# Kernel optimization log

Hardware: AMD Instinct MI355X
Metric: run time of the kernel (lower is better)

Reference implementation:

```python
import jax, jax.numpy as jnp
import numpy as np

N, E, DIN, DH, DOUT = 100000, 1600000, 512, 128, 40


def setup_inputs() -> dict:
    key = jax.random.key(0)
    ks = jax.random.split(key, 4)
    x = jax.random.normal(ks[0], (N, DIN), dtype=jnp.float32)
    edge_index = jax.random.randint(ks[1], (2, E), 0, N, dtype=jnp.int32)
    W1 = jax.random.normal(ks[2], (DIN, DH), dtype=jnp.float32) / np.sqrt(DIN).astype(np.float32)
    b1 = jnp.zeros((DH,), jnp.float32)
    W2 = jax.random.normal(ks[3], (DH, DOUT), dtype=jnp.float32) / np.sqrt(DH).astype(np.float32)
    b2 = jnp.zeros((DOUT,), jnp.float32)
    return {"x": x, "edge_index": edge_index, "W1": W1, "b1": b1, "W2": W2, "b2": b2}


def _gcn_conv(x, W, b, src, dst, norm, n):
    # PyG GCNConv: linear transform first, then normalized neighbor aggregation
    h = x @ W                                   # [n, d_out]
    msg = h[src] * norm[:, None]                # gather + scale, [E+n, d_out]
    out = jax.ops.segment_sum(msg, dst, num_segments=n)  # scatter-add
    return out + b


def reference(x, edge_index, W1, b1, W2, b2):
    n = x.shape[0]
    loops = jnp.arange(n, dtype=edge_index.dtype)
    src = jnp.concatenate([edge_index[0], loops])   # with self-loops
    dst = jnp.concatenate([edge_index[1], loops])
    deg = jax.ops.segment_sum(jnp.ones_like(dst, dtype=jnp.float32), dst, num_segments=n)
    dinv = jnp.where(deg > 0, jax.lax.rsqrt(jnp.maximum(deg, 1.0)), 0.0)
    norm = dinv[src] * dinv[dst]                    # deg^{-1/2}[j] * deg^{-1/2}[i]
    h = jax.nn.relu(_gcn_conv(x, W1, b1, src, dst, norm, n))
    # dropout p=0.5 is a no-op in eval mode (training=False)
    h = _gcn_conv(h, W2, b2, src, dst, norm, n)
    return h, jax.nn.log_softmax(h, axis=1)
```

## Files before the change

### kernel.cpp

```cpp
#include <hip/hip_runtime.h>
#include <math.h>


typedef unsigned int uint;
typedef unsigned short ushort_t;
using short8  = __attribute__((ext_vector_type(8))) short;
using float4v = __attribute__((ext_vector_type(4))) float;

__device__ __forceinline__ ushort_t f2bf(float f) {
    uint u = __float_as_uint(f);
    u += 0x7FFFu + ((u >> 16) & 1u);
    return (ushort_t)(u >> 16);
}
__device__ __forceinline__ float2 unpack2(uint v) {
    return make_float2(__uint_as_float(v << 16), __uint_as_float(v & 0xFFFF0000u));
}
__device__ __forceinline__ uint pack2(float a, float b) {
    return (uint)f2bf(a) | ((uint)f2bf(b) << 16);
}


__global__ __launch_bounds__(256) void k_bhist(const int* __restrict__ dst,
                                               int* __restrict__ bcnt, int e, int nb) {
    __shared__ int h[800];
    for (int t = threadIdx.x; t < nb; t += 256) h[t] = 0;
    __syncthreads();
    int ibase = blockIdx.x * 2560 + threadIdx.x;
#pragma unroll
    for (int j = 0; j < 10; j++) {
        int i = ibase + j * 256;
        if (i < e) atomicAdd(&h[dst[i] >> 7], 1);
    }
    __syncthreads();
    for (int t = threadIdx.x; t < nb; t += 256) {
        int c = h[t];
        if (c) atomicAdd(&bcnt[t], c);
    }
}

__global__ __launch_bounds__(256) void k_bscan(const int* __restrict__ bcnt, int* __restrict__ bbase,
                                               int* __restrict__ bcur, int* __restrict__ row_ptr,
                                               int nb, int n, int e) {
    __shared__ int sd[256];
    int t = threadIdx.x;
    int base = t * 4;
    int v[4];
#pragma unroll
    for (int j = 0; j < 4; j++) v[j] = (base + j < nb) ? bcnt[base + j] : 0;
    int s0 = v[0], s1 = s0 + v[1], s2 = s1 + v[2], s3 = s2 + v[3];
    sd[t] = s3;
    __syncthreads();
    for (int d = 1; d < 256; d <<= 1) {
        int x = (t >= d) ? sd[t - d] : 0;
        __syncthreads();
        sd[t] += x;
        __syncthreads();
    }
    int excl = sd[t] - s3;
    int pre0 = excl, pre1 = excl + s0, pre2 = excl + s1, pre3 = excl + s2;
    if (base + 0 < nb) { bbase[base + 0] = pre0; bcur[base + 0] = pre0; }
    if (base + 1 < nb) { bbase[base + 1] = pre1; bcur[base + 1] = pre1; }
    if (base + 2 < nb) { bbase[base + 2] = pre2; bcur[base + 2] = pre2; }
    if (base + 3 < nb) { bbase[base + 3] = pre3; bcur[base + 3] = pre3; }
    if (t == 255) bbase[nb] = excl + s3;
    if (t == 0) row_ptr[n] = e;
}

__global__ __launch_bounds__(256) void k_part(const int* __restrict__ src, const int* __restrict__ dst,
                                              int* __restrict__ bcur, uint* __restrict__ pbuf,
                                              int e, int nb) {
    __shared__ int h[800];
    __shared__ int base_l[800];
    for (int t = threadIdx.x; t < nb; t += 256) h[t] = 0;
    __syncthreads();
    uint pk[10]; int bk[10]; int lp[10];
    int ibase = blockIdx.x * 2560 + threadIdx.x;
#pragma unroll
    for (int j = 0; j < 10; j++) {
        int i = ibase + j * 256;
        bk[j] = -1;
        if (i < e) {
            int s = src[i], d = dst[i];
            int b = d >> 7;
            bk[j] = b;
            pk[j] = ((uint)(d & 127) << 25) | (uint)s;
            lp[j] = atomicAdd(&h[b], 1);
        }
    }
    __syncthreads();
    for (int t = threadIdx.x; t < nb; t += 256) {
        int c = h[t];
        base_l[t] = c ? atomicAdd(&bcur[t], c) : 0;
    }
    __syncthreads();
#pragma unroll
    for (int j = 0; j < 10; j++) {
        if (bk[j] >= 0) pbuf[base_l[bk[j]] + lp[j]] = pk[j];
    }
}

__global__ __launch_bounds__(256) void k_bsort(const uint* __restrict__ pbuf,
                                               const int* __restrict__ bbase,
                                               int* __restrict__ cnt,
                                               int* __restrict__ row_ptr,
                                               int* __restrict__ es_src, int n) {
    __shared__ int cl[128];
    __shared__ int cur[128];
    const int b = blockIdx.x;
    const int tid = threadIdx.x;
    const int ebeg = bbase[b], eend = bbase[b + 1];
    const int m = eend - ebeg;
    if (tid < 128) cl[tid] = 0;
    __syncthreads();
    for (int i = tid; i < m; i += 256) {
        uint p = pbuf[ebeg + i];
        atomicAdd(&cl[p >> 25], 1);
    }
    __syncthreads();
    int own = (tid < 128) ? cl[tid] : 0;
    for (int d = 1; d < 128; d <<= 1) {
        int v = 0;
        if (tid < 128 && tid >= d) v = cl[tid - d];
        __syncthreads();
        if (tid < 128 && tid >= d) cl[tid] += v;
        __syncthreads();
    }
    if (tid < 128) {
        int excl = cl[tid] - own;
        int node = b * 128 + tid;
        if (node < n) {
            cnt[node] = own;
            row_ptr[node] = ebeg + excl;
        }
        cur[tid] = excl;
    }
    __syncthreads();
    for (int i = tid; i < m; i += 256) {
        uint p = pbuf[ebeg + i];
        int dl = (int)(p >> 25);
        int pos = atomicAdd(&cur[dl], 1);
        es_src[ebeg + pos] = (int)(p & 0x1FFFFFFu);
    }
}

__global__ void k_dinv(const int* __restrict__ cnt, float* __restrict__ dinv, int n) {
    int i = blockIdx.x * blockDim.x + threadIdx.x;
    if (i < n) dinv[i] = rsqrtf((float)(cnt[i] + 1));
}

__global__ __launch_bounds__(256) void k_w1t(const float* __restrict__ W1, ushort_t* __restrict__ W1t) {
    int idx = blockIdx.x * 256 + threadIdx.x;
    int nn = idx >> 9, k = idx & 511;
    W1t[idx] = f2bf(W1[(size_t)k * 128 + nn]);
}

__global__ __launch_bounds__(256) void k_w2t(const float* __restrict__ W2, ushort_t* __restrict__ W2t) {
    int idx = blockIdx.x * 256 + threadIdx.x;
    if (idx >= 6144) return;
    int c = idx >> 7, k = idx & 127;
    W2t[idx] = (c < 40) ? f2bf(W2[(size_t)k * 40 + c]) : (ushort_t)0;
}

__global__ __launch_bounds__(256) void k_gemm1(const float* __restrict__ x,
                                               const ushort_t* __restrict__ W1t,
                                               const float* __restrict__ dinv,
                                               ushort_t* __restrict__ h, int n) {
    __shared__ ushort_t As[64][72];
    __shared__ ushort_t Bs[128][72];
    const int tid  = threadIdx.x;
    const int w    = tid >> 6, lane = tid & 63;
    const int quad = lane >> 4, l16 = lane & 15;
    const int row0 = blockIdx.x * 64;

    float4v acc[8];
#pragma unroll
    for (int i = 0; i < 8; i++) acc[i] = (float4v)0.f;

    const int ar  = tid >> 2;
    const int akq = (tid & 3) * 16;
    const int br  = tid >> 1;
    const int bkq = (tid & 1) * 32;
    const int agrow = row0 + ar;
    const float* xp0 = &x[(size_t)agrow * 512];
    const ushort_t* wp0 = &W1t[(size_t)br * 512];

    for (int kb = 0; kb < 512; kb += 64) {
#pragma unroll
        for (int j = 0; j < 4; j++) {
            float4 v = make_float4(0.f, 0.f, 0.f, 0.f);
            if (agrow < n) v = *(const float4*)(xp0 + kb + akq + j * 4);
            ushort4 b;
            b.x = f2bf(v.x); b.y = f2bf(v.y); b.z = f2bf(v.z); b.w = f2bf(v.w);
            *(ushort4*)&As[ar][akq + j * 4] = b;
        }
#pragma unroll
        for (int j = 0; j < 8; j++) {
            *(ushort4*)&Bs[br][bkq + j * 4] = *(const ushort4*)(wp0 + kb + bkq + j * 4);
        }
        __syncthreads();
#pragma unroll
        for (int ks = 0; ks < 64; ks += 32) {
            short8 a = *(const short8*)&As[w * 16 + l16][ks + quad * 8];
#pragma unroll
            for (int ct = 0; ct < 8; ct++) {
                short8 b = *(const short8*)&Bs[ct * 16 + l16][ks + quad * 8];
                acc[ct] = __builtin_amdgcn_mfma_f32_16x16x32_bf16(a, b, acc[ct], 0, 0, 0);
            }
        }
        __syncthreads();
    }
#pragma unroll
    for (int r = 0; r < 4; r++) {
        int grow = row0 + w * 16 + quad * 4 + r;
        if (grow >= n) continue;
        float di = dinv[grow];
#pragma unroll
        for (int ct = 0; ct < 8; ct++) {
            int col = ct * 16 + l16;
            h[(size_t)grow * 128 + col] = f2bf(di * acc[ct][r]);
        }
    }
}

__global__ __launch_bounds__(256) void k_agg1(const uint* __restrict__ h,
                                              const int* __restrict__ row_ptr,
                                              const int* __restrict__ es_src,
                                              const float* __restrict__ dinv,
                                              const float* __restrict__ b1,
                                              uint* __restrict__ h1, int n) {
    const int tid  = threadIdx.x;
    const int node = blockIdx.x * 4 + (tid >> 6);
    if (node >= n) return;
    const int lane = tid & 63;
    float2 acc = unpack2(h[(size_t)node * 64 + lane]);
    const int k0 = row_ptr[node], k1 = row_ptr[node + 1];
    int k = k0;
    for (; k + 3 < k1; k += 4) {
        int s0 = es_src[k], s1 = es_src[k + 1], s2 = es_src[k + 2], s3 = es_src[k + 3];
        float2 v0 = unpack2(h[(size_t)s0 * 64 + lane]);
        float2 v1 = unpack2(h[(size_t)s1 * 64 + lane]);
        float2 v2 = unpack2(h[(size_t)s2 * 64 + lane]);
        float2 v3 = unpack2(h[(size_t)s3 * 64 + lane]);
        acc.x += (v0.x + v1.x) + (v2.x + v3.x);
        acc.y += (v0.y + v1.y) + (v2.y + v3.y);
    }
    for (; k < k1; k++) {
        int s = es_src[k];
        float2 v = unpack2(h[(size_t)s * 64 + lane]);
        acc.x += v.x;
        acc.y += v.y;
    }
    const float di = dinv[node];
    float2 bb = *(const float2*)&b1[lane * 2];
    acc.x = di * acc.x + bb.x;
    acc.y = di * acc.y + bb.y;
    acc.x = acc.x > 0.f ? acc.x : 0.f;
    acc.y = acc.y > 0.f ? acc.y : 0.f;
    h1[(size_t)node * 64 + lane] = pack2(acc.x, acc.y);
}

__global__ __launch_bounds__(256) void k_gemm2(const ushort_t* __restrict__ h1,
                                               const ushort_t* __restrict__ W2t,
                                               const float* __restrict__ dinv,
                                               float* __restrict__ g, int n) {
    __shared__ ushort_t As[64][136];
    __shared__ ushort_t Bs[48][136];
    const int tid  = threadIdx.x;
    const int w    = tid >> 6, lane = tid & 63;
    const int quad = lane >> 4, l16 = lane & 15;
    const int row0 = blockIdx.x * 64;

    {
        int ar = tid >> 2;
        int ak = (tid & 3) * 32;
        int grow = row0 + ar;
#pragma unroll
        for (int j = 0; j < 4; j++) {
            uint4 v = make_uint4(0, 0, 0, 0);
            if (grow < n) v = *(const uint4*)&h1[(size_t)grow * 128 + ak + j * 8];
            *(uint4*)&As[ar][ak + j * 8] = v;
        }
    }
    for (int i = tid; i < 768; i += 256) {
        int row = i >> 4, q = i & 15;
        *(uint4*)&Bs[row][q * 8] = *(const uint4*)&W2t[(size_t)row * 128 + q * 8];
    }
    __syncthreads();

    float4v acc[3];
#pragma unroll
    for (int i = 0; i < 3; i++) acc[i] = (float4v)0.f;
#pragma unroll
    for (int ks = 0; ks < 128; ks += 32) {
        short8 a = *(const short8*)&As[w * 16 + l16][ks + quad * 8];
#pragma unroll
        for (int ct = 0; ct < 3; ct++) {
            short8 b = *(const short8*)&Bs[ct * 16 + l16][ks + quad * 8];
            acc[ct] = __builtin_amdgcn_mfma_f32_16x16x32_bf16(a, b, acc[ct], 0, 0, 0);
        }
    }
#pragma unroll
    for (int r = 0; r < 4; r++) {
        int grow = row0 + w * 16 + quad * 4 + r;
        if (grow >= n) continue;
        float di = dinv[grow];
#pragma unroll
        for (int ct = 0; ct < 3; ct++) {
            int col = ct * 16 + l16;
            if (col < 40) g[(size_t)grow * 40 + col] = di * acc[ct][r];
        }
    }
}

__global__ __launch_bounds__(256) void k_agg2f(const float* __restrict__ g,
                                               const int* __restrict__ row_ptr,
                                               const int* __restrict__ es_src,
                                               const float* __restrict__ dinv,
                                               const float* __restrict__ b2,
                                               float* __restrict__ out1,
                                               float* __restrict__ out2, int n) {
    __shared__ float s[6][40];
    __shared__ float mrow[6], lrow[6];
    const int tid = threadIdx.x;
    const int nl  = tid / 40;
    const int c   = tid % 40;
    const int node = blockIdx.x * 6 + nl;
    const bool active = (tid < 240) && (node < n);

    float v = 0.f;
    if (active) {
        float acc = g[(size_t)node * 40 + c];
        const int k0 = row_ptr[node], k1 = row_ptr[node + 1];
        int k = k0;
        for (; k + 3 < k1; k += 4) {
            int s0 = es_src[k], s1 = es_src[k + 1], s2 = es_src[k + 2], s3 = es_src[k + 3];
            float a0 = g[(size_t)s0 * 40 + c];
            float a1 = g[(size_t)s1 * 40 + c];
            float a2 = g[(size_t)s2 * 40 + c];
            float a3 = g[(size_t)s3 * 40 + c];
            acc += (a0 + a1) + (a2 + a3);
        }
        for (; k < k1; k++) acc += g[(size_t)es_src[k] * 40 + c];
        v = dinv[node] * acc + b2[c];
        s[nl][c] = v;
        out1[(size_t)node * 40 + c] = v;
    }
    __syncthreads();
    if (tid < 6 && blockIdx.x * 6 + tid < n) {
        float m = -1e30f;
        for (int k = 0; k < 40; k++) m = fmaxf(m, s[tid][k]);
        float sum = 0.f;
        for (int k = 0; k < 40; k++) sum += expf(s[tid][k] - m);
        mrow[tid] = m;
        lrow[tid] = logf(sum);
    }
    __syncthreads();
    if (active) out2[(size_t)node * 40 + c] = v - mrow[nl] - lrow[nl];
}

static inline size_t align4(size_t v) { return (v + 3) & ~(size_t)3; }

extern "C" void kernel_launch(void* const* d_in, const int* in_sizes, int n_in,
                              void* d_out, int out_size, void* d_ws, size_t ws_size,
                              hipStream_t stream) {
    const float* x  = (const float*)d_in[0];
    const int*   ei = (const int*)d_in[1];
    const float* W1 = (const float*)d_in[2];
    const float* b1 = (const float*)d_in[3];
    const float* W2 = (const float*)d_in[4];
    const float* b2 = (const float*)d_in[5];

    const int n = in_sizes[0] / 512;
    const int e = in_sizes[1] / 2;
    const int* src = ei;
    const int* dst = ei + e;
    const int NB = (n + 127) >> 7;

    char* p = (char*)d_ws;
    int*      bcnt    = (int*)p;        p += align4(NB) * 4;
    int*      bbase   = (int*)p;        p += align4(NB + 1) * 4;
    int*      bcur    = (int*)p;        p += align4(NB) * 4;
    int*      cnt     = (int*)p;        p += align4(n) * 4;
    int*      row_ptr = (int*)p;        p += align4(n + 1) * 4;
    float*    dinv    = (float*)p;      p += align4(n) * 4;
    uint*     pbuf    = (uint*)p;       p += align4(e) * 4;
    int*      es_src  = (int*)p;        p += align4(e) * 4;
    ushort_t* W1t     = (ushort_t*)p;   p += (size_t)128 * 512 * 2;
    ushort_t* W2t     = (ushort_t*)p;   p += (size_t)48 * 128 * 2;
    ushort_t* h       = (ushort_t*)p;   p += (size_t)n * 128 * 2;
    ushort_t* h1      = (ushort_t*)p;   p += (size_t)n * 128 * 2;
    float*    g       = (float*)h;
    float*    out1    = (float*)d_out;
    float*    out2    = out1 + (size_t)n * 40;

    const int B = 256;
    const int nblkA = (e + 2559) / 2560;

    hipMemsetAsync(bcnt, 0, (size_t)NB * 4, stream);
    k_bhist<<<nblkA, B, 0, stream>>>(dst, bcnt, e, NB);
    k_bscan<<<1, 256, 0, stream>>>(bcnt, bbase, bcur, row_ptr, NB, n, e);
    k_part<<<nblkA, B, 0, stream>>>(src, dst, bcur, pbuf, e, NB);
    k_bsort<<<NB, 256, 0, stream>>>(pbuf, bbase, cnt, row_ptr, es_src, n);
    k_dinv<<<(n + B - 1) / B, B, 0, stream>>>(cnt, dinv, n);

    k_w1t<<<256, 256, 0, stream>>>(W1, W1t);
    k_w2t<<<24, 256, 0, stream>>>(W2, W2t);

    k_gemm1<<<(n + 63) / 64, 256, 0, stream>>>(x, W1t, dinv, h, n);
    k_agg1<<<(n + 3) / 4, 256, 0, stream>>>((const uint*)h, row_ptr, es_src, dinv, b1, (uint*)h1, n);

    k_gemm2<<<(n + 63) / 64, 256, 0, stream>>>(h1, W2t, dinv, g, n);
    k_agg2f<<<(n + 5) / 6, 256, 0, stream>>>(g, row_ptr, es_src, dinv, b2, out1, out2, n);
}
```

Before: 572.4 us.

## Store layer-2 features as padded bf16 and rewrite aggregation with wave-level softmax

The layer-2 GEMM now writes its projected features as bf16 padded to 64 columns instead of fp32 with 40 columns. The second aggregation is rewritten to use one wavefront per node: each half-wave gathers alternate edges with 32-bit loads, the halves are combined with shuffles, and log_softmax is done with wave shuffles instead of shared memory. The dinv computation is folded into the bucket sort, and the two weight-transpose kernels are merged into one, removing launches. This aims to halve gather bandwidth in the second aggregation and cut launch overhead, at the cost of bf16 rounding in the layer-2 messages.

```diff
diff --git a/kernel.cpp b/kernel.cpp
--- a/kernel.cpp
+++ b/kernel.cpp
@@ -101,7 +101,7 @@
 
 __global__ __launch_bounds__(256) void k_bsort(const uint* __restrict__ pbuf,
                                                const int* __restrict__ bbase,
-                                               int* __restrict__ cnt,
+                                               float* __restrict__ dinv,
                                                int* __restrict__ row_ptr,
                                                int* __restrict__ es_src, int n) {
     __shared__ int cl[128];
@@ -129,7 +129,7 @@
         int excl = cl[tid] - own;
         int node = b * 128 + tid;
         if (node < n) {
-            cnt[node] = own;
+            dinv[node] = rsqrtf((float)(own + 1));
             row_ptr[node] = ebeg + excl;
         }
         cur[tid] = excl;
@@ -143,22 +143,21 @@
     }
 }
 
-__global__ void k_dinv(const int* __restrict__ cnt, float* __restrict__ dinv, int n) {
-    int i = blockIdx.x * blockDim.x + threadIdx.x;
-    if (i < n) dinv[i] = rsqrtf((float)(cnt[i] + 1));
-}
-
-__global__ __launch_bounds__(256) void k_w1t(const float* __restrict__ W1, ushort_t* __restrict__ W1t) {
+__global__ __launch_bounds__(256) void k_wprep(const float* __restrict__ W1,
+                                               const float* __restrict__ W2,
+                                               ushort_t* __restrict__ W1t,
+                                               ushort_t* __restrict__ W2t) {
     int idx = blockIdx.x * 256 + threadIdx.x;
-    int nn = idx >> 9, k = idx & 511;
-    W1t[idx] = f2bf(W1[(size_t)k * 128 + nn]);
-}
-
-__global__ __launch_bounds__(256) void k_w2t(const float* __restrict__ W2, ushort_t* __restrict__ W2t) {
-    int idx = blockIdx.x * 256 + threadIdx.x;
-    if (idx >= 6144) return;
-    int c = idx >> 7, k = idx & 127;
-    W2t[idx] = (c < 40) ? f2bf(W2[(size_t)k * 40 + c]) : (ushort_t)0;
+    if (idx < 65536) {
+        int nn = idx >> 9, k = idx & 511;
+        W1t[idx] = f2bf(W1[(size_t)k * 128 + nn]);
+    } else {
+        int j = idx - 65536;
+        if (j < 6144) {
+            int c = j >> 7, k = j & 127;
+            W2t[j] = (c < 40) ? f2bf(W2[(size_t)k * 40 + c]) : (ushort_t)0;
+        }
+    }
 }
 
 __global__ __launch_bounds__(256) void k_gemm1(const float* __restrict__ x,
@@ -262,7 +261,7 @@
 __global__ __launch_bounds__(256) void k_gemm2(const ushort_t* __restrict__ h1,
                                                const ushort_t* __restrict__ W2t,
                                                const float* __restrict__ dinv,
-                                               float* __restrict__ g, int n) {
+                                               ushort_t* __restrict__ g, int n) {
     __shared__ ushort_t As[64][136];
     __shared__ ushort_t Bs[48][136];
     const int tid  = threadIdx.x;
@@ -307,55 +306,62 @@
 #pragma unroll
         for (int ct = 0; ct < 3; ct++) {
             int col = ct * 16 + l16;
-            if (col < 40) g[(size_t)grow * 40 + col] = di * acc[ct][r];
-        }
-    }
-}
-
-__global__ __launch_bounds__(256) void k_agg2f(const float* __restrict__ g,
-                                               const int* __restrict__ row_ptr,
-                                               const int* __restrict__ es_src,
-                                               const float* __restrict__ dinv,
-                                               const float* __restrict__ b2,
-                                               float* __restrict__ out1,
-                                               float* __restrict__ out2, int n) {
-    __shared__ float s[6][40];
-    __shared__ float mrow[6], lrow[6];
-    const int tid = threadIdx.x;
-    const int nl  = tid / 40;
-    const int c   = tid % 40;
-    const int node = blockIdx.x * 6 + nl;
-    const bool active = (tid < 240) && (node < n);
-
-    float v = 0.f;
-    if (active) {
-        float acc = g[(size_t)node * 40 + c];
-        const int k0 = row_ptr[node], k1 = row_ptr[node + 1];
-        int k = k0;
-        for (; k + 3 < k1; k += 4) {
-            int s0 = es_src[k], s1 = es_src[k + 1], s2 = es_src[k + 2], s3 = es_src[k + 3];
-            float a0 = g[(size_t)s0 * 40 + c];
-            float a1 = g[(size_t)s1 * 40 + c];
-            float a2 = g[(size_t)s2 * 40 + c];
-            float a3 = g[(size_t)s3 * 40 + c];
-            acc += (a0 + a1) + (a2 + a3);
-        }
-        for (; k < k1; k++) acc += g[(size_t)es_src[k] * 40 + c];
-        v = dinv[node] * acc + b2[c];
-        s[nl][c] = v;
-        out1[(size_t)node * 40 + c] = v;
-    }
-    __syncthreads();
-    if (tid < 6 && blockIdx.x * 6 + tid < n) {
-        float m = -1e30f;
-        for (int k = 0; k < 40; k++) m = fmaxf(m, s[tid][k]);
-        float sum = 0.f;
-        for (int k = 0; k < 40; k++) sum += expf(s[tid][k] - m);
-        mrow[tid] = m;
-        lrow[tid] = logf(sum);
-    }
-    __syncthreads();
-    if (active) out2[(size_t)node * 40 + c] = v - mrow[nl] - lrow[nl];
+            g[(size_t)grow * 64 + col] = f2bf(di * acc[ct][r]);
+        }
+        g[(size_t)grow * 64 + 48 + l16] = (ushort_t)0;
+    }
+}
+
+__global__ __launch_bounds__(256) void k_agg2(const uint* __restrict__ g,
+                                              const int* __restrict__ row_ptr,
+                                              const int* __restrict__ es_src,
+                                              const float* __restrict__ dinv,
+                                              const float* __restrict__ b2,
+                                              float* __restrict__ out1,
+                                              float* __restrict__ out2, int n) {
+    const int tid  = threadIdx.x;
+    const int node = blockIdx.x * 4 + (tid >> 6);
+    if (node >= n) return;
+    const int lane = tid & 63;
+    const int half = lane >> 5;
+    const int l    = lane & 31;
+
+    float2 acc = make_float2(0.f, 0.f);
+    if (half == 0) acc = unpack2(g[(size_t)node * 32 + l]);
+    const int k0 = row_ptr[node], k1 = row_ptr[node + 1];
+    int k = k0 + half;
+    for (; k + 2 < k1; k += 4) {
+        int s0 = es_src[k], s1 = es_src[k + 2];
+        float2 v0 = unpack2(g[(size_t)s0 * 32 + l]);
+        float2 v1 = unpack2(g[(size_t)s1 * 32 + l]);
+        acc.x += v0.x + v1.x;
+        acc.y += v0.y + v1.y;
+    }
+    for (; k < k1; k += 2) {
+        float2 v = unpack2(g[(size_t)es_src[k] * 32 + l]);
+        acc.x += v.x;
+        acc.y += v.y;
+    }
+    acc.x += __shfl_xor(acc.x, 32);
+    acc.y += __shfl_xor(acc.y, 32);
+
+    const float di = dinv[node];
+    float2 bb = (l < 20) ? *(const float2*)&b2[l * 2] : make_float2(0.f, 0.f);
+    float v0 = di * acc.x + bb.x;
+    float v1 = di * acc.y + bb.y;
+
+    float m = (l < 20) ? fmaxf(v0, v1) : -1e30f;
+#pragma unroll
+    for (int d = 16; d; d >>= 1) m = fmaxf(m, __shfl_xor(m, d));
+    float s = (l < 20) ? (expf(v0 - m) + expf(v1 - m)) : 0.f;
+#pragma unroll
+    for (int d = 16; d; d >>= 1) s += __shfl_xor(s, d);
+    float ls = logf(s) + m;
+
+    if (half == 0 && l < 20) {
+        *(float2*)&out1[(size_t)node * 40 + l * 2] = make_float2(v0, v1);
+        *(float2*)&out2[(size_t)node * 40 + l * 2] = make_float2(v0 - ls, v1 - ls);
+    }
 }
 
 static inline size_t align4(size_t v) { return (v + 3) & ~(size_t)3; }
@@ -380,7 +386,6 @@
     int*      bcnt    = (int*)p;        p += align4(NB) * 4;
     int*      bbase   = (int*)p;        p += align4(NB + 1) * 4;
     int*      bcur    = (int*)p;        p += align4(NB) * 4;
-    int*      cnt     = (int*)p;        p += align4(n) * 4;
     int*      row_ptr = (int*)p;        p += align4(n + 1) * 4;
     float*    dinv    = (float*)p;      p += align4(n) * 4;
     uint*     pbuf    = (uint*)p;       p += align4(e) * 4;
@@ -389,7 +394,7 @@
     ushort_t* W2t     = (ushort_t*)p;   p += (size_t)48 * 128 * 2;
     ushort_t* h       = (ushort_t*)p;   p += (size_t)n * 128 * 2;
     ushort_t* h1      = (ushort_t*)p;   p += (size_t)n * 128 * 2;
-    float*    g       = (float*)h;
+    ushort_t* g       = h;
     float*    out1    = (float*)d_out;
     float*    out2    = out1 + (size_t)n * 40;
 
@@ -400,15 +405,13 @@
     k_bhist<<<nblkA, B, 0, stream>>>(dst, bcnt, e, NB);
     k_bscan<<<1, 256, 0, stream>>>(bcnt, bbase, bcur, row_ptr, NB, n, e);
     k_part<<<nblkA, B, 0, stream>>>(src, dst, bcur, pbuf, e, NB);
-    k_bsort<<<NB, 256, 0, stream>>>(pbuf, bbase, cnt, row_ptr, es_src, n);
-    k_dinv<<<(n + B - 1) / B, B, 0, stream>>>(cnt, dinv, n);
-
-    k_w1t<<<256, 256, 0, stream>>>(W1, W1t);
-    k_w2t<<<24, 256, 0, stream>>>(W2, W2t);
+    k_bsort<<<NB, 256, 0, stream>>>(pbuf, bbase, dinv, row_ptr, es_src, n);
+
+    k_wprep<<<280, 256, 0, stream>>>(W1, W2, W1t, W2t);
 
     k_gemm1<<<(n + 63) / 64, 256, 0, stream>>>(x, W1t, dinv, h, n);
     k_agg1<<<(n + 3) / 4, 256, 0, stream>>>((const uint*)h, row_ptr, es_src, dinv, b1, (uint*)h1, n);
 
     k_gemm2<<<(n + 63) / 64, 256, 0, stream>>>(h1, W2t, dinv, g, n);
-    k_agg2f<<<(n + 5) / 6, 256, 0, stream>>>(g, row_ptr, es_src, dinv, b2, out1, out2, n);
-}
+    k_agg2<<<(n + 3) / 4, 256, 0, stream>>>((const uint*)g, row_ptr, es_src, dinv, b2, out1, out2, n);
+}
```

Result: faster. 560.6 us (-2.1%).
